# Kernel optimization log

Hardware: AMD Instinct MI355X
Metric: run time of the kernel (lower is better)

The kernel has to match this reference:

```python
import jax, jax.numpy as jnp
import numpy as np

N_HEAD = 16
D_K = 128
D_MODEL = N_HEAD * D_K  # 2048


def setup_inputs() -> dict:
    key = jax.random.key(0)
    ks = jax.random.split(key, 12)
    bs, q_len, kv_len = 32, 16, 2048
    scale = 1.0 / np.sqrt(D_MODEL)
    inp = {
        "x": jax.random.normal(ks[0], (bs, q_len, D_MODEL), jnp.float32),
        "k_cache": jax.random.normal(ks[1], (bs, kv_len, D_MODEL), jnp.float32),
        "v_cache": jax.random.normal(ks[2], (bs, kv_len, D_MODEL), jnp.float32),
        "mask": jnp.ones((bs, q_len, kv_len), jnp.int32),
        "Wq": jax.random.normal(ks[3], (D_MODEL, D_MODEL), jnp.float32) * scale,
        "bq": jnp.zeros((D_MODEL,), jnp.float32),
        "Wk": jax.random.normal(ks[4], (D_MODEL, D_MODEL), jnp.float32) * scale,
        "bk": jnp.zeros((D_MODEL,), jnp.float32),
        "Wv": jax.random.normal(ks[5], (D_MODEL, D_MODEL), jnp.float32) * scale,
        "bv": jnp.zeros((D_MODEL,), jnp.float32),
        "Wo": jax.random.normal(ks[6], (D_MODEL, D_MODEL), jnp.float32) * scale,
        "bo": jnp.zeros((D_MODEL,), jnp.float32),
    }
    return inp


def reference(x, k_cache, v_cache, mask, Wq, bq, Wk, bk, Wv, bv, Wo, bo):
    bs, q_len, d_model = x.shape
    # QKV projections (nn.Linear => x @ W.T + b)
    q = x @ Wq.T + bq
    k = x @ Wk.T + bk
    v = x @ Wv.T + bv
    # KV-cache slice write at the last q_len positions
    k_cache = k_cache.at[:, -q_len:, :].set(k)
    v_cache = v_cache.at[:, -q_len:, :].set(v)
    # split heads: [b, s, h, dk] -> [b, h, s, dk]
    qh = q.reshape(bs, q_len, N_HEAD, D_K).transpose(0, 2, 1, 3)
    kh = k_cache.reshape(bs, -1, N_HEAD, D_K).transpose(0, 2, 1, 3)
    vh = v_cache.reshape(bs, -1, N_HEAD, D_K).transpose(0, 2, 1, 3)
    # scaled dot-product attention with mask broadcast over heads
    scores = jnp.einsum("bhqd,bhkd->bhqk", qh, kh) / np.sqrt(D_K)
    scores = jnp.where(mask[:, None, :, :] == 0, jnp.float32(-1e9), scores)
    attn = jax.nn.softmax(scores, axis=-1)
    out = jnp.einsum("bhqk,bhkd->bhqd", attn, vh)
    out = out.transpose(0, 2, 1, 3).reshape(bs, q_len, d_model)
    # output projection (dropout is identity at inference)
    out = out @ Wo.T + bo
    return (out, k_cache, v_cache)
```

## Files before the change

### kernel.cpp

```cpp
#include <hip/hip_runtime.h>
#include <hip/hip_bf16.h>

#define BS 32
#define QL 16
#define KV 2048
#define NH 16
#define DK 128
#define DM 2048
#define MROWS (BS*QL)
#define KCA 4
#define AROWS (KV/KCA)
#define KCB 2
#define BROWS (KV/KCB)
#define SPLICE (KV-QL)

#define SCALE 0.08838834764831845f
#define LOG2E 1.4426950408889634f

typedef __bf16 bf16x8 __attribute__((ext_vector_type(8)));
typedef float f32x4 __attribute__((ext_vector_type(4)));
typedef unsigned short us8 __attribute__((ext_vector_type(8)));
typedef unsigned short us4 __attribute__((ext_vector_type(4)));

__device__ inline unsigned short f2bf(float f){
    unsigned u = __builtin_bit_cast(unsigned, f);
    u += 0x7fffu + ((u >> 16) & 1u);
    return (unsigned short)(u >> 16);
}
__device__ inline float bf2f(unsigned short u){
    unsigned x = ((unsigned)u) << 16;
    return __builtin_bit_cast(float, x);
}

__global__ __launch_bounds__(256) void gemm_bt(
    const float* __restrict__ A, const float* __restrict__ A2,
    const float* __restrict__ W0, const float* __restrict__ W1, const float* __restrict__ W2,
    const float* __restrict__ b0, const float* __restrict__ b1, const float* __restrict__ b2,
    float* __restrict__ C0, float* __restrict__ C1, float* __restrict__ C2,
    int spliceMask)
{
    int z = blockIdx.z;
    const float* W    = (z==0)?W0:(z==1)?W1:W2;
    const float* bias = (z==0)?b0:(z==1)?b1:b2;
    float*       C    = (z==0)?C0:(z==1)?C1:C2;
    int spl = (spliceMask >> z) & 1;

    const int K = DM, N = DM;
    int mBase = blockIdx.x * 64, nBase = blockIdx.y * 64;

    __shared__ __align__(16) unsigned short As[64*40];
    __shared__ __align__(16) unsigned short Bs[64*40];

    int t = threadIdx.x;
    int wv = t >> 6, lane = t & 63;
    int row = t >> 2, seg = (t & 3) * 8;
    int g = lane >> 4, c = lane & 15;

    f32x4 acc[4] = {{0,0,0,0},{0,0,0,0},{0,0,0,0},{0,0,0,0}};

    for (int k0 = 0; k0 < K; k0 += 32) {
        __syncthreads();
        {
            const float* ap = A + (size_t)(mBase + row) * K + k0 + seg;
            float4 a0 = *(const float4*)ap, a1 = *(const float4*)(ap + 4);
            if (A2) {
                const float* ap2 = A2 + (size_t)(mBase + row) * K + k0 + seg;
                float4 c0 = *(const float4*)ap2, c1 = *(const float4*)(ap2 + 4);
                a0.x+=c0.x; a0.y+=c0.y; a0.z+=c0.z; a0.w+=c0.w;
                a1.x+=c1.x; a1.y+=c1.y; a1.z+=c1.z; a1.w+=c1.w;
            }
            us8 av = { f2bf(a0.x), f2bf(a0.y), f2bf(a0.z), f2bf(a0.w),
                       f2bf(a1.x), f2bf(a1.y), f2bf(a1.z), f2bf(a1.w) };
            *(us8*)&As[row*40 + seg] = av;
        }
        {
            const float* wp = W + (size_t)(nBase + row) * K + k0 + seg;
            float4 w0v = *(const float4*)wp, w1v = *(const float4*)(wp + 4);
            us8 wv8 = { f2bf(w0v.x), f2bf(w0v.y), f2bf(w0v.z), f2bf(w0v.w),
                        f2bf(w1v.x), f2bf(w1v.y), f2bf(w1v.z), f2bf(w1v.w) };
            *(us8*)&Bs[row*40 + seg] = wv8;
        }
        __syncthreads();

        bf16x8 af = __builtin_bit_cast(bf16x8, *(us8*)&As[(wv*16 + c)*40 + g*8]);
        #pragma unroll
        for (int j = 0; j < 4; j++) {
            bf16x8 bf = __builtin_bit_cast(bf16x8, *(us8*)&Bs[(j*16 + c)*40 + g*8]);
            acc[j] = __builtin_amdgcn_mfma_f32_16x16x32_bf16(af, bf, acc[j], 0, 0, 0);
        }
    }

    #pragma unroll
    for (int j = 0; j < 4; j++) {
        int n = nBase + j*16 + c;
        float bb = bias[n];
        #pragma unroll
        for (int r = 0; r < 4; r++) {
            int m = mBase + wv*16 + g*4 + r;
            size_t rowoff = spl ? ((size_t)(m >> 4) * KV + SPLICE + (m & 15)) * (size_t)N
                                : (size_t)m * (size_t)N;
            C[rowoff + n] = acc[j][r] + bb;
        }
    }
}

__global__ __launch_bounds__(256) void kcopy_scores(
    const float* __restrict__ qws, const float* __restrict__ kcache,
    const int* __restrict__ mask,
    float* __restrict__ kout, __hip_bfloat16* __restrict__ Sbuf,
    float* __restrict__ statsM, float* __restrict__ statsL)
{
    int h = blockIdx.x, b = blockIdx.y, kc = blockIdx.z;
    int t = threadIdx.x, wv = t >> 6, lane = t & 63;
    int g = lane >> 4, c = lane & 15;
    size_t bKV = (size_t)b * KV;
    size_t bh  = (size_t)b * NH + h;
    unsigned short* S = (unsigned short*)Sbuf;

    __shared__ float smM[4][16], smL[4][16];

    bf16x8 af[4];
    {
        const float* qp = qws + (size_t)(b*QL + c) * DM + h*DK + g*8;
        #pragma unroll
        for (int ks = 0; ks < 4; ks++) {
            float4 q0 = *(const float4*)(qp + ks*32);
            float4 q1 = *(const float4*)(qp + ks*32 + 4);
            us8 qv = { f2bf(q0.x*SCALE), f2bf(q0.y*SCALE), f2bf(q0.z*SCALE), f2bf(q0.w*SCALE),
                       f2bf(q1.x*SCALE), f2bf(q1.y*SCALE), f2bf(q1.z*SCALE), f2bf(q1.w*SCALE) };
            af[ks] = __builtin_bit_cast(bf16x8, qv);
        }
    }

    float mloc[4] = {-1e30f,-1e30f,-1e30f,-1e30f};
    float lloc[4] = {0.f,0.f,0.f,0.f};

    for (int i = 0; i < 8; i++) {
        int n0 = kc*AROWS + (i*4 + wv)*16;
        int krow = n0 + c;
        bool spl = (n0 >= SPLICE);
        const float* src = (spl ? kout : kcache) + (bKV + krow)*DM + h*DK + g*8;

        float4 kvv[8];
        #pragma unroll
        for (int ks = 0; ks < 4; ks++) {
            kvv[2*ks]   = *(const float4*)(src + ks*32);
            kvv[2*ks+1] = *(const float4*)(src + ks*32 + 4);
        }
        if (!spl) {
            float* dst = kout + (bKV + krow)*DM + h*DK + g*8;
            #pragma unroll
            for (int ks = 0; ks < 4; ks++) {
                *(float4*)(dst + ks*32)     = kvv[2*ks];
                *(float4*)(dst + ks*32 + 4) = kvv[2*ks+1];
            }
        }
        f32x4 sc = {0,0,0,0};
        #pragma unroll
        for (int ks = 0; ks < 4; ks++) {
            float4 k0 = kvv[2*ks], k1 = kvv[2*ks+1];
            us8 kb = { f2bf(k0.x), f2bf(k0.y), f2bf(k0.z), f2bf(k0.w),
                       f2bf(k1.x), f2bf(k1.y), f2bf(k1.z), f2bf(k1.w) };
            sc = __builtin_amdgcn_mfma_f32_16x16x32_bf16(af[ks],
                    __builtin_bit_cast(bf16x8, kb), sc, 0, 0, 0);
        }
        const int* mrow = mask + (size_t)b * QL * KV + krow;
        us4 sv;
        #pragma unroll
        for (int r = 0; r < 4; r++) {
            int q = g*4 + r;
            float s = sc[r];
            if (mrow[(size_t)q * KV] == 0) s = -1e9f;
            unsigned short u = f2bf(s);
            sv[r] = u;
            float sb = bf2f(u);
            float nm = fmaxf(mloc[r], sb);
            lloc[r] = lloc[r]*exp2f((mloc[r]-nm)*LOG2E) + exp2f((sb-nm)*LOG2E);
            mloc[r] = nm;
        }
        *(us4*)(void*)&S[(bh*KV + krow)*QL + g*4] = sv;
    }

    #pragma unroll
    for (int r = 0; r < 4; r++) {
        float m = mloc[r], l = lloc[r];
        #pragma unroll
        for (int mm = 1; mm < 16; mm <<= 1) {
            float mo = __shfl_xor(m, mm), lo = __shfl_xor(l, mm);
            float nm = fmaxf(m, mo);
            l = l*exp2f((m-nm)*LOG2E) + lo*exp2f((mo-nm)*LOG2E);
            m = nm;
        }
        if (c == 0) { smM[wv][g*4+r] = m; smL[wv][g*4+r] = l; }
    }
    __syncthreads();
    if (t < 16) {
        float M = -1e30f;
        #pragma unroll
        for (int w = 0; w < 4; w++) M = fmaxf(M, smM[w][t]);
        float L = 0.f;
        #pragma unroll
        for (int w = 0; w < 4; w++) L += smL[w][t]*exp2f((smM[w][t]-M)*LOG2E);
        statsM[(bh*KCA + kc)*QL + t] = M;
        statsL[(bh*KCA + kc)*QL + t] = L;
    }
}

__global__ __launch_bounds__(256) void vcopy_pv(
    const float* __restrict__ vcache, const __hip_bfloat16* __restrict__ Sbuf,
    const float* __restrict__ statsM, const float* __restrict__ statsL,
    float* __restrict__ vout, float* __restrict__ awsP)
{
    int hd = blockIdx.x; int h = hd >> 1, half = hd & 1;
    int b = blockIdx.y, kc = blockIdx.z;
    int t = threadIdx.x;
    size_t bKV = (size_t)b * KV;
    size_t bh  = (size_t)b * NH + h;
    const unsigned short* S = (const unsigned short*)Sbuf;

    __shared__ float smM[16], smLinv[16];
    __shared__ __align__(16) unsigned short Vl[64*72];
    __shared__ __align__(16) float Pl[16*68];

    if (t < 16) {
        float M = -1e30f;
        #pragma unroll
        for (int c4 = 0; c4 < KCA; c4++)
            M = fmaxf(M, statsM[(bh*KCA + c4)*QL + t]);
        float L = 0.f;
        #pragma unroll
        for (int c4 = 0; c4 < KCA; c4++)
            L += statsL[(bh*KCA + c4)*QL + t]*exp2f((statsM[(bh*KCA + c4)*QL + t]-M)*LOG2E);
        smM[t] = M; smLinv[t] = 1.0f / L;
    }
    __syncthreads();

    int q = t >> 4, dc = t & 15;
    int srow = t >> 2;
    int vseg = (t & 3) * 16;
    int pq0  = (t & 3) * 4;

    float O[4] = {0.f,0.f,0.f,0.f};

    for (int kt = 0; kt < 16; kt++) {
        int k0 = kc*BROWS + kt*64;
        __syncthreads();
        {
            int krow = k0 + srow;
            us4 sv = *(const us4*)(const void*)&S[(bh*KV + krow)*QL + pq0];
            #pragma unroll
            for (int j = 0; j < 4; j++)
                Pl[(pq0+j)*68 + srow] = exp2f((bf2f(sv[j]) - smM[pq0+j])*LOG2E);
        }
        {
            int vrow = k0 + srow;
            bool cpy = (vrow < SPLICE);
            const float* src = (cpy ? vcache : vout) + (bKV + vrow)*DM + h*DK + half*64 + vseg;
            float4 v0 = *(const float4*)(src);
            float4 v1 = *(const float4*)(src + 4);
            float4 v2 = *(const float4*)(src + 8);
            float4 v3 = *(const float4*)(src + 12);
            if (cpy) {
                float* dst = vout + (bKV + vrow)*DM + h*DK + half*64 + vseg;
                *(float4*)(dst)      = v0;
                *(float4*)(dst + 4)  = v1;
                *(float4*)(dst + 8)  = v2;
                *(float4*)(dst + 12) = v3;
            }
            us8 p0 = { f2bf(v0.x), f2bf(v0.y), f2bf(v0.z), f2bf(v0.w),
                       f2bf(v1.x), f2bf(v1.y), f2bf(v1.z), f2bf(v1.w) };
            us8 p1 = { f2bf(v2.x), f2bf(v2.y), f2bf(v2.z), f2bf(v2.w),
                       f2bf(v3.x), f2bf(v3.y), f2bf(v3.z), f2bf(v3.w) };
            *(us8*)&Vl[srow*72 + vseg]     = p0;
            *(us8*)&Vl[srow*72 + vseg + 8] = p1;
        }
        __syncthreads();
        #pragma unroll
        for (int kk0 = 0; kk0 < 64; kk0 += 4) {
            float4 pv = *(const float4*)&Pl[q*68 + kk0];
            #pragma unroll
            for (int j = 0; j < 4; j++) {
                us4 vb = *(const us4*)(const void*)&Vl[(kk0+j)*72 + dc*4];
                float pj = pv[j];
                O[0] += pj*bf2f(vb[0]); O[1] += pj*bf2f(vb[1]);
                O[2] += pj*bf2f(vb[2]); O[3] += pj*bf2f(vb[3]);
            }
        }
    }

    float inv = smLinv[q];
    float* op = awsP + (size_t)kc * MROWS * DM
              + (size_t)(b*QL + q)*DM + h*DK + half*64 + dc*4;
    float4 ov = {O[0]*inv, O[1]*inv, O[2]*inv, O[3]*inv};
    *(float4*)op = ov;
}

extern "C" void kernel_launch(void* const* d_in, const int* in_sizes, int n_in,
                              void* d_out, int out_size, void* d_ws, size_t ws_size,
                              hipStream_t stream)
{
    (void)in_sizes; (void)n_in; (void)out_size; (void)ws_size;

    const float* x      = (const float*)d_in[0];
    const float* kcache = (const float*)d_in[1];
    const float* vcache = (const float*)d_in[2];
    const int*   mask   = (const int*)  d_in[3];
    const float* Wq     = (const float*)d_in[4];
    const float* bq     = (const float*)d_in[5];
    const float* Wk     = (const float*)d_in[6];
    const float* bk     = (const float*)d_in[7];
    const float* Wv     = (const float*)d_in[8];
    const float* bv     = (const float*)d_in[9];
    const float* Wo     = (const float*)d_in[10];
    const float* bo     = (const float*)d_in[11];

    float* out  = (float*)d_out;
    float* kout = out  + (size_t)MROWS * DM;
    float* vout = kout + (size_t)BS * KV * DM;

    float* qws    = (float*)d_ws;
    float* aws0   = qws  + (size_t)MROWS * DM;
    float* aws1   = aws0 + (size_t)MROWS * DM;
    float* statsM = aws1 + (size_t)MROWS * DM;
    float* statsL = statsM + (size_t)BS * NH * KCA * QL;
    __hip_bfloat16* Sbuf = (__hip_bfloat16*)(statsL + (size_t)BS * NH * KCA * QL);

    dim3 gq(MROWS/64, DM/64, 3);
    gemm_bt<<<gq, 256, 0, stream>>>(x, nullptr, Wq, Wk, Wv, bq, bk, bv,
                                    qws, kout, vout, 0b110);

    dim3 ga(NH, BS, KCA);
    kcopy_scores<<<ga, 256, 0, stream>>>(qws, kcache, mask, kout, Sbuf, statsM, statsL);

    dim3 gb(NH*2, BS, KCB);
    vcopy_pv<<<gb, 256, 0, stream>>>(vcache, Sbuf, statsM, statsL, vout, aws0);

    dim3 go(MROWS/64, DM/64, 1);
    gemm_bt<<<go, 256, 0, stream>>>(aws0, aws1, Wo, Wo, Wo, bo, bo, bo,
                                    out, out, out, 0);
}
```

Measured before the change: 635.8 us.

## Stage K/V tiles through LDS across four heads with contiguous row loads

The K-score and V-weighted-sum kernels now give each block a group of four heads (512 contiguous floats per cache row). A 32-row tile is loaded with fully coalesced float4 reads, copied into the output cache, converted to bf16 into a swizzled LDS buffer, and each wave works on its own head. The KV split factors grow to 8 and 4, so the output projection GEMM now sums four partial buffers. The aim is better global coalescing for the dominant cache copy and read traffic. In exchange it adds 32 KB of LDS per block, fewer blocks per (batch, chunk), and more partial-sum reads in the final GEMM.

After: 745.5 us. 17.2% more time.

```diff
diff --git a/kernel.cpp b/kernel.cpp
--- a/kernel.cpp
+++ b/kernel.cpp
@@ -8,9 +8,9 @@
 #define DK 128
 #define DM 2048
 #define MROWS (BS*QL)
-#define KCA 4
+#define KCA 8
 #define AROWS (KV/KCA)
-#define KCB 2
+#define KCB 4
 #define BROWS (KV/KCB)
 #define SPLICE (KV-QL)
 
@@ -33,7 +33,8 @@
 }
 
 __global__ __launch_bounds__(256) void gemm_bt(
-    const float* __restrict__ A, const float* __restrict__ A2,
+    const float* __restrict__ A0p, const float* __restrict__ A1p,
+    const float* __restrict__ A2p, const float* __restrict__ A3p,
     const float* __restrict__ W0, const float* __restrict__ W1, const float* __restrict__ W2,
     const float* __restrict__ b0, const float* __restrict__ b1, const float* __restrict__ b2,
     float* __restrict__ C0, float* __restrict__ C1, float* __restrict__ C2,
@@ -61,11 +62,20 @@
     for (int k0 = 0; k0 < K; k0 += 32) {
         __syncthreads();
         {
-            const float* ap = A + (size_t)(mBase + row) * K + k0 + seg;
-            float4 a0 = *(const float4*)ap, a1 = *(const float4*)(ap + 4);
-            if (A2) {
-                const float* ap2 = A2 + (size_t)(mBase + row) * K + k0 + seg;
-                float4 c0 = *(const float4*)ap2, c1 = *(const float4*)(ap2 + 4);
+            size_t off = (size_t)(mBase + row) * K + k0 + seg;
+            float4 a0 = *(const float4*)(A0p + off), a1 = *(const float4*)(A0p + off + 4);
+            if (A1p) {
+                float4 c0 = *(const float4*)(A1p + off), c1 = *(const float4*)(A1p + off + 4);
+                a0.x+=c0.x; a0.y+=c0.y; a0.z+=c0.z; a0.w+=c0.w;
+                a1.x+=c1.x; a1.y+=c1.y; a1.z+=c1.z; a1.w+=c1.w;
+            }
+            if (A2p) {
+                float4 c0 = *(const float4*)(A2p + off), c1 = *(const float4*)(A2p + off + 4);
+                a0.x+=c0.x; a0.y+=c0.y; a0.z+=c0.z; a0.w+=c0.w;
+                a1.x+=c1.x; a1.y+=c1.y; a1.z+=c1.z; a1.w+=c1.w;
+            }
+            if (A3p) {
+                float4 c0 = *(const float4*)(A3p + off), c1 = *(const float4*)(A3p + off + 4);
                 a0.x+=c0.x; a0.y+=c0.y; a0.z+=c0.z; a0.w+=c0.w;
                 a1.x+=c1.x; a1.y+=c1.y; a1.z+=c1.z; a1.w+=c1.w;
             }
@@ -110,14 +120,15 @@
     float* __restrict__ kout, __hip_bfloat16* __restrict__ Sbuf,
     float* __restrict__ statsM, float* __restrict__ statsL)
 {
-    int h = blockIdx.x, b = blockIdx.y, kc = blockIdx.z;
+    int hg = blockIdx.x, b = blockIdx.y, kc = blockIdx.z;
     int t = threadIdx.x, wv = t >> 6, lane = t & 63;
     int g = lane >> 4, c = lane & 15;
+    int h = hg*4 + wv;
     size_t bKV = (size_t)b * KV;
     size_t bh  = (size_t)b * NH + h;
     unsigned short* S = (unsigned short*)Sbuf;
 
-    __shared__ float smM[4][16], smL[4][16];
+    __shared__ __align__(16) unsigned short Kl[32*512];
 
     bf16x8 af[4];
     {
@@ -135,55 +146,57 @@
     float mloc[4] = {-1e30f,-1e30f,-1e30f,-1e30f};
     float lloc[4] = {0.f,0.f,0.f,0.f};
 
-    for (int i = 0; i < 8; i++) {
-        int n0 = kc*AROWS + (i*4 + wv)*16;
-        int krow = n0 + c;
-        bool spl = (n0 >= SPLICE);
-        const float* src = (spl ? kout : kcache) + (bKV + krow)*DM + h*DK + g*8;
-
-        float4 kvv[8];
-        #pragma unroll
-        for (int ks = 0; ks < 4; ks++) {
-            kvv[2*ks]   = *(const float4*)(src + ks*32);
-            kvv[2*ks+1] = *(const float4*)(src + ks*32 + 4);
-        }
-        if (!spl) {
-            float* dst = kout + (bKV + krow)*DM + h*DK + g*8;
+    for (int tile = 0; tile < AROWS/32; ++tile) {
+        int row0 = kc*AROWS + tile*32;
+        __syncthreads();
+        #pragma unroll
+        for (int p = 0; p < 16; p++) {
+            int f = p*256 + t;
+            int r = f >> 7;
+            int d4 = (f & 127) * 4;
+            int grow = row0 + r;
+            size_t off = (bKV + grow)*DM + hg*512 + d4;
+            const float* src = (grow >= SPLICE ? kout : kcache) + off;
+            float4 v = *(const float4*)src;
+            if (grow < SPLICE) *(float4*)(kout + off) = v;
+            int e = (r*512 + d4) ^ ((r & 7) << 3);
+            us4 bv = { f2bf(v.x), f2bf(v.y), f2bf(v.z), f2bf(v.w) };
+            *(us4*)&Kl[e] = bv;
+        }
+        __syncthreads();
+
+        #pragma unroll
+        for (int sub = 0; sub < 2; ++sub) {
+            int r = sub*16 + c;
+            f32x4 sc = {0,0,0,0};
             #pragma unroll
             for (int ks = 0; ks < 4; ks++) {
-                *(float4*)(dst + ks*32)     = kvv[2*ks];
-                *(float4*)(dst + ks*32 + 4) = kvv[2*ks+1];
-            }
-        }
-        f32x4 sc = {0,0,0,0};
-        #pragma unroll
-        for (int ks = 0; ks < 4; ks++) {
-            float4 k0 = kvv[2*ks], k1 = kvv[2*ks+1];
-            us8 kb = { f2bf(k0.x), f2bf(k0.y), f2bf(k0.z), f2bf(k0.w),
-                       f2bf(k1.x), f2bf(k1.y), f2bf(k1.z), f2bf(k1.w) };
-            sc = __builtin_amdgcn_mfma_f32_16x16x32_bf16(af[ks],
-                    __builtin_bit_cast(bf16x8, kb), sc, 0, 0, 0);
-        }
-        const int* mrow = mask + (size_t)b * QL * KV + krow;
-        us4 sv;
-        #pragma unroll
-        for (int r = 0; r < 4; r++) {
-            int q = g*4 + r;
-            float s = sc[r];
-            if (mrow[(size_t)q * KV] == 0) s = -1e9f;
-            unsigned short u = f2bf(s);
-            sv[r] = u;
-            float sb = bf2f(u);
-            float nm = fmaxf(mloc[r], sb);
-            lloc[r] = lloc[r]*exp2f((mloc[r]-nm)*LOG2E) + exp2f((sb-nm)*LOG2E);
-            mloc[r] = nm;
-        }
-        *(us4*)(void*)&S[(bh*KV + krow)*QL + g*4] = sv;
+                int e = (r*512 + wv*128 + ks*32 + g*8) ^ ((r & 7) << 3);
+                sc = __builtin_amdgcn_mfma_f32_16x16x32_bf16(af[ks],
+                        __builtin_bit_cast(bf16x8, *(us8*)&Kl[e]), sc, 0, 0, 0);
+            }
+            int krow = row0 + sub*16 + c;
+            const int* mrow = mask + (size_t)b * QL * KV + krow;
+            us4 sv;
+            #pragma unroll
+            for (int rr = 0; rr < 4; rr++) {
+                int q = g*4 + rr;
+                float s = sc[rr];
+                if (mrow[(size_t)q * KV] == 0) s = -1e9f;
+                unsigned short u = f2bf(s);
+                sv[rr] = u;
+                float sb = bf2f(u);
+                float nm = fmaxf(mloc[rr], sb);
+                lloc[rr] = lloc[rr]*exp2f((mloc[rr]-nm)*LOG2E) + exp2f((sb-nm)*LOG2E);
+                mloc[rr] = nm;
+            }
+            *(us4*)(void*)&S[(bh*KV + krow)*QL + g*4] = sv;
+        }
     }
 
     #pragma unroll
-    for (int r = 0; r < 4; r++) {
-        float m = mloc[r], l = lloc[r];
+    for (int rr = 0; rr < 4; rr++) {
+        float m = mloc[rr], l = lloc[rr];
         #pragma unroll
         for (int mm = 1; mm < 16; mm <<= 1) {
             float mo = __shfl_xor(m, mm), lo = __shfl_xor(l, mm);
@@ -191,18 +204,10 @@
             l = l*exp2f((m-nm)*LOG2E) + lo*exp2f((mo-nm)*LOG2E);
             m = nm;
         }
-        if (c == 0) { smM[wv][g*4+r] = m; smL[wv][g*4+r] = l; }
-    }
-    __syncthreads();
-    if (t < 16) {
-        float M = -1e30f;
-        #pragma unroll
-        for (int w = 0; w < 4; w++) M = fmaxf(M, smM[w][t]);
-        float L = 0.f;
-        #pragma unroll
-        for (int w = 0; w < 4; w++) L += smL[w][t]*exp2f((smM[w][t]-M)*LOG2E);
-        statsM[(bh*KCA + kc)*QL + t] = M;
-        statsL[(bh*KCA + kc)*QL + t] = L;
+        if (c == 0) {
+            statsM[(bh*KCA + kc)*QL + g*4 + rr] = m;
+            statsL[(bh*KCA + kc)*QL + g*4 + rr] = l;
+        }
     }
 }
 
@@ -211,88 +216,88 @@
     const float* __restrict__ statsM, const float* __restrict__ statsL,
     float* __restrict__ vout, float* __restrict__ awsP)
 {
-    int hd = blockIdx.x; int h = hd >> 1, half = hd & 1;
-    int b = blockIdx.y, kc = blockIdx.z;
-    int t = threadIdx.x;
+    int dg = blockIdx.x, b = blockIdx.y, kc = blockIdx.z;
+    int t = threadIdx.x, wv = t >> 6, lane = t & 63;
+    int h = dg*4 + wv;
     size_t bKV = (size_t)b * KV;
     size_t bh  = (size_t)b * NH + h;
     const unsigned short* S = (const unsigned short*)Sbuf;
 
-    __shared__ float smM[16], smLinv[16];
-    __shared__ __align__(16) unsigned short Vl[64*72];
-    __shared__ __align__(16) float Pl[16*68];
-
-    if (t < 16) {
+    __shared__ __align__(16) unsigned short Vl[32*512];
+    __shared__ float Pl[4][32][17];
+    __shared__ float sM[4][16], sLinv[4][16];
+
+    if (t < 64) {
+        int hh = t >> 4, q = t & 15;
+        size_t bhh = (size_t)b*NH + dg*4 + hh;
         float M = -1e30f;
         #pragma unroll
-        for (int c4 = 0; c4 < KCA; c4++)
-            M = fmaxf(M, statsM[(bh*KCA + c4)*QL + t]);
+        for (int c8 = 0; c8 < KCA; c8++)
+            M = fmaxf(M, statsM[(bhh*KCA + c8)*QL + q]);
         float L = 0.f;
         #pragma unroll
-        for (int c4 = 0; c4 < KCA; c4++)
-            L += statsL[(bh*KCA + c4)*QL + t]*exp2f((statsM[(bh*KCA + c4)*QL + t]-M)*LOG2E);
-        smM[t] = M; smLinv[t] = 1.0f / L;
+        for (int c8 = 0; c8 < KCA; c8++)
+            L += statsL[(bhh*KCA + c8)*QL + q] * exp2f((statsM[(bhh*KCA + c8)*QL + q] - M)*LOG2E);
+        sM[hh][q] = M; sLinv[hh][q] = 1.0f / L;
     }
     __syncthreads();
 
-    int q = t >> 4, dc = t & 15;
-    int srow = t >> 2;
-    int vseg = (t & 3) * 16;
-    int pq0  = (t & 3) * 4;
-
-    float O[4] = {0.f,0.f,0.f,0.f};
-
-    for (int kt = 0; kt < 16; kt++) {
-        int k0 = kc*BROWS + kt*64;
+    int q = lane >> 2, dq = lane & 3;
+    float O[32];
+    #pragma unroll
+    for (int i = 0; i < 32; i++) O[i] = 0.f;
+
+    for (int tile = 0; tile < BROWS/32; ++tile) {
+        int row0 = kc*BROWS + tile*32;
         __syncthreads();
         {
-            int krow = k0 + srow;
-            us4 sv = *(const us4*)(const void*)&S[(bh*KV + krow)*QL + pq0];
+            int idx = t & 63;
+            int k = idx >> 1, q0 = (idx & 1) * 8;
+            int krow = row0 + k;
+            us8 sv = *(const us8*)(const void*)&S[(bh*KV + krow)*QL + q0];
             #pragma unroll
-            for (int j = 0; j < 4; j++)
-                Pl[(pq0+j)*68 + srow] = exp2f((bf2f(sv[j]) - smM[pq0+j])*LOG2E);
-        }
-        {
-            int vrow = k0 + srow;
-            bool cpy = (vrow < SPLICE);
-            const float* src = (cpy ? vcache : vout) + (bKV + vrow)*DM + h*DK + half*64 + vseg;
-            float4 v0 = *(const float4*)(src);
-            float4 v1 = *(const float4*)(src + 4);
-            float4 v2 = *(const float4*)(src + 8);
-            float4 v3 = *(const float4*)(src + 12);
-            if (cpy) {
-                float* dst = vout + (bKV + vrow)*DM + h*DK + half*64 + vseg;
-                *(float4*)(dst)      = v0;
-                *(float4*)(dst + 4)  = v1;
-                *(float4*)(dst + 8)  = v2;
-                *(float4*)(dst + 12) = v3;
-            }
-            us8 p0 = { f2bf(v0.x), f2bf(v0.y), f2bf(v0.z), f2bf(v0.w),
-                       f2bf(v1.x), f2bf(v1.y), f2bf(v1.z), f2bf(v1.w) };
-            us8 p1 = { f2bf(v2.x), f2bf(v2.y), f2bf(v2.z), f2bf(v2.w),
-                       f2bf(v3.x), f2bf(v3.y), f2bf(v3.z), f2bf(v3.w) };
-            *(us8*)&Vl[srow*72 + vseg]     = p0;
-            *(us8*)&Vl[srow*72 + vseg + 8] = p1;
-        }
-        __syncthreads();
-        #pragma unroll
-        for (int kk0 = 0; kk0 < 64; kk0 += 4) {
-            float4 pv = *(const float4*)&Pl[q*68 + kk0];
+            for (int j = 0; j < 8; j++)
+                Pl[wv][k][q0 + j] = exp2f((bf2f(sv[j]) - sM[wv][q0 + j])*LOG2E);
+        }
+        #pragma unroll
+        for (int p = 0; p < 16; p++) {
+            int f = p*256 + t;
+            int r = f >> 7;
+            int d4 = (f & 127) * 4;
+            int grow = row0 + r;
+            size_t off = (bKV + grow)*DM + dg*512 + d4;
+            const float* src = (grow >= SPLICE ? vout : vcache) + off;
+            float4 v = *(const float4*)src;
+            if (grow < SPLICE) *(float4*)(vout + off) = v;
+            int e = (r*512 + d4) ^ ((r & 7) << 3);
+            us4 bv = { f2bf(v.x), f2bf(v.y), f2bf(v.z), f2bf(v.w) };
+            *(us4*)&Vl[e] = bv;
+        }
+        __syncthreads();
+        for (int k = 0; k < 32; k++) {
+            float p = Pl[wv][k][q];
             #pragma unroll
             for (int j = 0; j < 4; j++) {
-                us4 vb = *(const us4*)(const void*)&Vl[(kk0+j)*72 + dc*4];
-                float pj = pv[j];
-                O[0] += pj*bf2f(vb[0]); O[1] += pj*bf2f(vb[1]);
-                O[2] += pj*bf2f(vb[2]); O[3] += pj*bf2f(vb[3]);
-            }
-        }
-    }
-
-    float inv = smLinv[q];
+                int e = (k*512 + wv*128 + dq*32 + j*8) ^ ((k & 7) << 3);
+                us8 v8 = *(const us8*)&Vl[e];
+                O[j*8+0] += p*bf2f(v8[0]); O[j*8+1] += p*bf2f(v8[1]);
+                O[j*8+2] += p*bf2f(v8[2]); O[j*8+3] += p*bf2f(v8[3]);
+                O[j*8+4] += p*bf2f(v8[4]); O[j*8+5] += p*bf2f(v8[5]);
+                O[j*8+6] += p*bf2f(v8[6]); O[j*8+7] += p*bf2f(v8[7]);
+            }
+        }
+    }
+
+    float inv = sLinv[wv][q];
     float* op = awsP + (size_t)kc * MROWS * DM
-              + (size_t)(b*QL + q)*DM + h*DK + half*64 + dc*4;
-    float4 ov = {O[0]*inv, O[1]*inv, O[2]*inv, O[3]*inv};
-    *(float4*)op = ov;
+              + (size_t)(b*QL + q)*DM + dg*512 + wv*128 + dq*32;
+    #pragma unroll
+    for (int j = 0; j < 4; j++) {
+        float4 o0 = {O[j*8+0]*inv, O[j*8+1]*inv, O[j*8+2]*inv, O[j*8+3]*inv};
+        float4 o1 = {O[j*8+4]*inv, O[j*8+5]*inv, O[j*8+6]*inv, O[j*8+7]*inv};
+        *(float4*)(op + j*8)     = o0;
+        *(float4*)(op + j*8 + 4) = o1;
+    }
 }
 
 extern "C" void kernel_launch(void* const* d_in, const int* in_sizes, int n_in,
@@ -319,23 +324,28 @@
     float* vout = kout + (size_t)BS * KV * DM;
 
     float* qws    = (float*)d_ws;
-    float* aws0   = qws  + (size_t)MROWS * DM;
-    float* aws1   = aws0 + (size_t)MROWS * DM;
-    float* statsM = aws1 + (size_t)MROWS * DM;
+    float* awsP   = qws  + (size_t)MROWS * DM;
+    float* statsM = awsP + (size_t)KCB * MROWS * DM;
     float* statsL = statsM + (size_t)BS * NH * KCA * QL;
     __hip_bfloat16* Sbuf = (__hip_bfloat16*)(statsL + (size_t)BS * NH * KCA * QL);
 
     dim3 gq(MROWS/64, DM/64, 3);
-    gemm_bt<<<gq, 256, 0, stream>>>(x, nullptr, Wq, Wk, Wv, bq, bk, bv,
+    gemm_bt<<<gq, 256, 0, stream>>>(x, nullptr, nullptr, nullptr,
+                                    Wq, Wk, Wv, bq, bk, bv,
                                     qws, kout, vout, 0b110);
 
-    dim3 ga(NH, BS, KCA);
+    dim3 ga(4, BS, KCA);
     kcopy_scores<<<ga, 256, 0, stream>>>(qws, kcache, mask, kout, Sbuf, statsM, statsL);
 
-    dim3 gb(NH*2, BS, KCB);
-    vcopy_pv<<<gb, 256, 0, stream>>>(vcache, Sbuf, statsM, statsL, vout, aws0);
-
+    dim3 gb(4, BS, KCB);
+    vcopy_pv<<<gb, 256, 0, stream>>>(vcache, Sbuf, statsM, statsL, vout, awsP);
+
+    float* a0 = awsP;
+    float* a1 = awsP + 1*(size_t)MROWS*DM;
+    float* a2 = awsP + 2*(size_t)MROWS*DM;
+    float* a3 = awsP + 3*(size_t)MROWS*DM;
     dim3 go(MROWS/64, DM/64, 1);
-    gemm_bt<<<go, 256, 0, stream>>>(aws0, aws1, Wo, Wo, Wo, bo, bo, bo,
+    gemm_bt<<<go, 256, 0, stream>>>(a0, a1, a2, a3,
+                                    Wo, Wo, Wo, bo, bo, bo,
                                     out, out, out, 0);
 }
```
